# Kernel tuning notes

Measured on AMD Instinct MI355X. Metric: run time of the kernel, lower is better.

The kernel has to match this reference:

```python
import jax, jax.numpy as jnp
import numpy as np
from jax import lax

K = 16      # number of neighbors (init k)
TEMP = 1.0  # softmax temperature (init temp)
DIM = 256   # key/query dim (init dim)


def _compute_omega(s, k, t):
    # s: [*B, N]. Faithful port of the torch loop:
    #   alpha = softmax(s); omega_0 = softmax(alpha/t)
    #   alpha += log(1 - omega_{i-1}); omega_i = softmax(alpha/t)
    alpha0 = jax.nn.softmax(s, axis=-1)

    def step(alpha, _):
        om = jax.nn.softmax(alpha / t, axis=-1)
        return alpha + jnp.log(1.0 - om), om

    _, omegas = lax.scan(step, alpha0, None, length=k)  # [K, *B, N]
    return jnp.moveaxis(omegas, 0, -1)  # [*B, N, K]


def setup_inputs() -> dict:
    key = jax.random.key(0)
    kq, kk, kv = jax.random.split(key, 3)
    B, D, N, F = 8, DIM, 32768, 256
    query = jax.random.normal(kq, (B, D), dtype=jnp.float32)
    keys = jax.random.normal(kk, (B, D, N), dtype=jnp.float32)
    values = jax.random.normal(kv, (B, F, N), dtype=jnp.float32)
    return {"query": query, "keys": keys, "values": values}


def reference(query, keys, values):
    # similarity: -(q . k) / sqrt(D)  -> [B, N]
    sims = -jnp.einsum('bd,bdn->bn', query, keys) / (DIM ** 0.5)
    omega = _compute_omega(sims, K, TEMP)  # [B, N, K]
    # weighted aggregation of values -> [B, K, F]
    k_nearest = jnp.einsum('bnk,bfn->bkf', omega, values)
    return k_nearest
```

## Files before the change

### kernel.cpp

```cpp
#include <hip/hip_runtime.h>

#define B_ 8
#define D_ 256
#define N_ 32768
#define F_ 256
#define K_ 16

__global__ __launch_bounds__(1024) void sims_kernel(
    const float* __restrict__ q, const float* __restrict__ keys,
    float* __restrict__ sims) {
  const int b = blockIdx.x >> 5;
  const int chunk = blockIdx.x & 31;
  const int t = threadIdx.x;
  const int c = t & 255;
  const int g = t >> 8;
  __shared__ float qs[D_];
  __shared__ float4 part[4][256];
  if (t < D_) qs[t] = q[b * D_ + t];
  __syncthreads();
  const int n0 = chunk * 1024 + c * 4;
  const float* kp = keys + (size_t)b * D_ * N_ + (size_t)(g * 64) * N_ + n0;
  const float* qg = qs + g * 64;
  float ax = 0.f, ay = 0.f, az = 0.f, aw = 0.f;
#pragma unroll 8
  for (int d = 0; d < 64; ++d) {
    float4 kv = *reinterpret_cast<const float4*>(kp + (size_t)d * N_);
    float qd = qg[d];
    ax += qd * kv.x; ay += qd * kv.y; az += qd * kv.z; aw += qd * kv.w;
  }
  part[g][c] = make_float4(ax, ay, az, aw);
  __syncthreads();
  if (g == 0) {
    float4 p1 = part[1][c], p2 = part[2][c], p3 = part[3][c];
    float4 o;
    o.x = -0.0625f * (ax + p1.x + p2.x + p3.x);
    o.y = -0.0625f * (ay + p1.y + p2.y + p3.y);
    o.z = -0.0625f * (az + p1.z + p2.z + p3.z);
    o.w = -0.0625f * (aw + p1.w + p2.w + p3.w);
    *reinterpret_cast<float4*>(sims + (size_t)b * N_ + n0) = o;
  }
}

__device__ __forceinline__ float block_allreduce(float v, bool is_max,
                                                 float* red) {
  const int t = threadIdx.x;
#pragma unroll
  for (int off = 32; off > 0; off >>= 1) {
    float o = __shfl_xor(v, off, 64);
    v = is_max ? fmaxf(v, o) : (v + o);
  }
  __syncthreads();
  if ((t & 63) == 0) red[t >> 6] = v;
  __syncthreads();
  if (t == 0) {
    float x = red[0];
#pragma unroll
    for (int w = 1; w < 16; ++w) x = is_max ? fmaxf(x, red[w]) : (x + red[w]);
    red[16] = x;
  }
  __syncthreads();
  return red[16];
}

__global__ __launch_bounds__(1024) void stats_kernel(
    const float* __restrict__ sims, float* __restrict__ om,
    float* __restrict__ qout) {
  const int b = blockIdx.x;
  const int t = threadIdx.x;
  const float* s = sims + (size_t)b * N_;
  float* ob = om + (size_t)b * N_;
  __shared__ float red[17];

  float a[32];
#pragma unroll
  for (int j = 0; j < 32; ++j) a[j] = s[t + j * 1024];

  float m = -1e30f;
#pragma unroll
  for (int j = 0; j < 32; ++j) m = fmaxf(m, a[j]);
  m = block_allreduce(m, true, red);

  float sum = 0.f;
#pragma unroll
  for (int j = 0; j < 32; ++j) { a[j] = __expf(a[j] - m); sum += a[j]; }
  const float invZ1 = 1.0f / block_allreduce(sum, false, red);

  float s1 = 0.f, s2 = 0.f;
#pragma unroll
  for (int j = 0; j < 32; ++j) {
    float f = __expf(a[j] * invZ1);
    a[j] = f;
    s1 += f;
    s2 += f * f;
  }
  const float Z2 = block_allreduce(s1, false, red);
  const float S2 = block_allreduce(s2, false, red);
  const float invZ2 = 1.0f / Z2;
#pragma unroll
  for (int j = 0; j < 32; ++j) ob[t + j * 1024] = a[j] * invZ2;
  if (t == 0) qout[b] = S2 * invZ2 * invZ2;
}

__global__ __launch_bounds__(256) void agg_kernel(
    const float* __restrict__ om, const float* __restrict__ values,
    const float* __restrict__ qarr, float* __restrict__ out) {
  const int b = blockIdx.x & 7;
  const int f0 = (blockIdx.x >> 3) * 4;
  const int t = threadIdx.x;
  const float* ob = om + (size_t)b * N_;
  const float* vb = values + (size_t)b * F_ * N_;

  float A[4] = {0.f, 0.f, 0.f, 0.f};
  float Bv[4] = {0.f, 0.f, 0.f, 0.f};

#pragma unroll 2
  for (int it = 0; it < 32; ++it) {
    const int n0 = (it * 256 + t) * 4;
    float4 o4 = *reinterpret_cast<const float4*>(ob + n0);
    float4 o2;
    o2.x = o4.x * o4.x; o2.y = o4.y * o4.y;
    o2.z = o4.z * o4.z; o2.w = o4.w * o4.w;
#pragma unroll
    for (int f = 0; f < 4; ++f) {
      float4 v4 = *reinterpret_cast<const float4*>(vb + (size_t)(f0 + f) * N_ + n0);
      A[f]  += v4.x * o4.x + v4.y * o4.y + v4.z * o4.z + v4.w * o4.w;
      Bv[f] += v4.x * o2.x + v4.y * o2.y + v4.z * o2.z + v4.w * o2.w;
    }
  }

#pragma unroll
  for (int f = 0; f < 4; ++f) {
#pragma unroll
    for (int off = 32; off > 0; off >>= 1) {
      A[f]  += __shfl_xor(A[f], off, 64);
      Bv[f] += __shfl_xor(Bv[f], off, 64);
    }
  }

  __shared__ float red[4][8];
  const int wid = t >> 6, lane = t & 63;
  if (lane == 0) {
#pragma unroll
    for (int f = 0; f < 4; ++f) { red[wid][f] = A[f]; red[wid][4 + f] = Bv[f]; }
  }
  __syncthreads();
  if (t < 64) {
    const int k = t & 15, fi = t >> 4;
    const float Af = red[0][fi] + red[1][fi] + red[2][fi] + red[3][fi];
    const float Bf = red[0][4 + fi] + red[1][4 + fi] + red[2][4 + fi] + red[3][4 + fi];
    const float qb = qarr[b];
    out[((size_t)b * K_ + k) * F_ + f0 + fi] = Af + (float)k * (qb * Af - Bf);
  }
}

extern "C" void kernel_launch(void* const* d_in, const int* in_sizes, int n_in,
                              void* d_out, int out_size, void* d_ws, size_t ws_size,
                              hipStream_t stream) {
  const float* q = (const float*)d_in[0];
  const float* keys = (const float*)d_in[1];
  const float* values = (const float*)d_in[2];
  float* out = (float*)d_out;
  float* ws = (float*)d_ws;
  float* sims = ws;
  float* om   = ws + (size_t)B_ * N_;
  float* qarr = ws + (size_t)2 * B_ * N_;

  sims_kernel<<<dim3(256), dim3(1024), 0, stream>>>(q, keys, sims);
  stats_kernel<<<dim3(B_), dim3(1024), 0, stream>>>(sims, om, qarr);
  agg_kernel<<<dim3(512), dim3(256), 0, stream>>>(om, values, qarr, out);
}
```

Baseline: 108.7 us.

## Replace softmax stats kernel with Taylor-moment expansion fused into sims and aggregation

Removes the single-block-per-batch stats kernel by computing exp(sims) and its partial moment sums (sum e, e^2, e^3) directly in the similarity kernel. The aggregation kernel accumulates value sums weighted by e^0..e^3 and reconstructs the second softmax and its correction term through a third-order Taylor expansion in double precision. This eliminates the serialized low-parallelism stats pass and one workspace round trip. The trade-off is that accuracy relies on the second-softmax inputs (alpha ~ 1/N) being small enough for the truncated series, and the aggregation does more FMAs per value load.

```diff
diff --git a/kernel.cpp b/kernel.cpp
--- a/kernel.cpp
+++ b/kernel.cpp
@@ -6,19 +6,23 @@
 #define F_ 256
 #define K_ 16
 
-__global__ __launch_bounds__(1024) void sims_kernel(
+
+__device__ __forceinline__ float sum4(float4 v) { return v.x + v.y + v.z + v.w; }
+
+__global__ __launch_bounds__(512) void expsim_kernel(
     const float* __restrict__ q, const float* __restrict__ keys,
-    float* __restrict__ sims) {
-  const int b = blockIdx.x >> 5;
-  const int chunk = blockIdx.x & 31;
+    float* __restrict__ e, float* __restrict__ pp) {
+  const int b = blockIdx.x >> 6;
+  const int chunk = blockIdx.x & 63;
   const int t = threadIdx.x;
-  const int c = t & 255;
-  const int g = t >> 8;
+  const int c = t & 127;
+  const int g = t >> 7;
   __shared__ float qs[D_];
-  __shared__ float4 part[4][256];
+  __shared__ float4 part[3][128];
+  __shared__ float pr[8][3];
   if (t < D_) qs[t] = q[b * D_ + t];
   __syncthreads();
-  const int n0 = chunk * 1024 + c * 4;
+  const int n0 = chunk * 512 + c * 4;
   const float* kp = keys + (size_t)b * D_ * N_ + (size_t)(g * 64) * N_ + n0;
   const float* qg = qs + g * 64;
   float ax = 0.f, ay = 0.f, az = 0.f, aw = 0.f;
@@ -28,128 +32,131 @@
     float qd = qg[d];
     ax += qd * kv.x; ay += qd * kv.y; az += qd * kv.z; aw += qd * kv.w;
   }
-  part[g][c] = make_float4(ax, ay, az, aw);
+  if (g > 0) part[g - 1][c] = make_float4(ax, ay, az, aw);
   __syncthreads();
+  float s1 = 0.f, s2 = 0.f, s3 = 0.f;
   if (g == 0) {
-    float4 p1 = part[1][c], p2 = part[2][c], p3 = part[3][c];
-    float4 o;
-    o.x = -0.0625f * (ax + p1.x + p2.x + p3.x);
-    o.y = -0.0625f * (ay + p1.y + p2.y + p3.y);
-    o.z = -0.0625f * (az + p1.z + p2.z + p3.z);
-    o.w = -0.0625f * (aw + p1.w + p2.w + p3.w);
-    *reinterpret_cast<float4*>(sims + (size_t)b * N_ + n0) = o;
+    float4 p1 = part[0][c], p2 = part[1][c], p3 = part[2][c];
+    float4 ev;
+    ev.x = __expf(-0.0625f * (ax + p1.x + p2.x + p3.x));
+    ev.y = __expf(-0.0625f * (ay + p1.y + p2.y + p3.y));
+    ev.z = __expf(-0.0625f * (az + p1.z + p2.z + p3.z));
+    ev.w = __expf(-0.0625f * (aw + p1.w + p2.w + p3.w));
+    *reinterpret_cast<float4*>(e + (size_t)b * N_ + n0) = ev;
+    float4 e2 = make_float4(ev.x * ev.x, ev.y * ev.y, ev.z * ev.z, ev.w * ev.w);
+    s1 = sum4(ev);
+    s2 = sum4(e2);
+    s3 = e2.x * ev.x + e2.y * ev.y + e2.z * ev.z + e2.w * ev.w;
+  }
+#pragma unroll
+  for (int off = 32; off > 0; off >>= 1) {
+    s1 += __shfl_xor(s1, off, 64);
+    s2 += __shfl_xor(s2, off, 64);
+    s3 += __shfl_xor(s3, off, 64);
+  }
+  if ((t & 63) == 0) { pr[t >> 6][0] = s1; pr[t >> 6][1] = s2; pr[t >> 6][2] = s3; }
+  __syncthreads();
+  if (t == 0) {
+    float r1 = 0.f, r2 = 0.f, r3 = 0.f;
+#pragma unroll
+    for (int w = 0; w < 8; ++w) { r1 += pr[w][0]; r2 += pr[w][1]; r3 += pr[w][2]; }
+    pp[0 * B_ * 64 + b * 64 + chunk] = r1;
+    pp[1 * B_ * 64 + b * 64 + chunk] = r2;
+    pp[2 * B_ * 64 + b * 64 + chunk] = r3;
   }
 }
 
-__device__ __forceinline__ float block_allreduce(float v, bool is_max,
-                                                 float* red) {
+__global__ __launch_bounds__(256, 4) void agg_kernel(
+    const float* __restrict__ e, const float* __restrict__ values,
+    const float* __restrict__ pp, float* __restrict__ out) {
+  const int b = blockIdx.x & 7;
+  const int f0 = (blockIdx.x >> 3) * 2;
   const int t = threadIdx.x;
+  const float* eb = e + (size_t)b * N_;
+  const float* vp0 = values + ((size_t)b * F_ + f0) * N_;
+  const float* vp1 = vp0 + N_;
+
+  float4 a0[2], a1[2], a2[2], a3[2];
 #pragma unroll
-  for (int off = 32; off > 0; off >>= 1) {
-    float o = __shfl_xor(v, off, 64);
-    v = is_max ? fmaxf(v, o) : (v + o);
+  for (int f = 0; f < 2; ++f) {
+    a0[f] = make_float4(0, 0, 0, 0); a1[f] = make_float4(0, 0, 0, 0);
+    a2[f] = make_float4(0, 0, 0, 0); a3[f] = make_float4(0, 0, 0, 0);
   }
-  __syncthreads();
-  if ((t & 63) == 0) red[t >> 6] = v;
-  __syncthreads();
-  if (t == 0) {
-    float x = red[0];
-#pragma unroll
-    for (int w = 1; w < 16; ++w) x = is_max ? fmaxf(x, red[w]) : (x + red[w]);
-    red[16] = x;
-  }
-  __syncthreads();
-  return red[16];
-}
-
-__global__ __launch_bounds__(1024) void stats_kernel(
-    const float* __restrict__ sims, float* __restrict__ om,
-    float* __restrict__ qout) {
-  const int b = blockIdx.x;
-  const int t = threadIdx.x;
-  const float* s = sims + (size_t)b * N_;
-  float* ob = om + (size_t)b * N_;
-  __shared__ float red[17];
-
-  float a[32];
-#pragma unroll
-  for (int j = 0; j < 32; ++j) a[j] = s[t + j * 1024];
-
-  float m = -1e30f;
-#pragma unroll
-  for (int j = 0; j < 32; ++j) m = fmaxf(m, a[j]);
-  m = block_allreduce(m, true, red);
-
-  float sum = 0.f;
-#pragma unroll
-  for (int j = 0; j < 32; ++j) { a[j] = __expf(a[j] - m); sum += a[j]; }
-  const float invZ1 = 1.0f / block_allreduce(sum, false, red);
-
-  float s1 = 0.f, s2 = 0.f;
-#pragma unroll
-  for (int j = 0; j < 32; ++j) {
-    float f = __expf(a[j] * invZ1);
-    a[j] = f;
-    s1 += f;
-    s2 += f * f;
-  }
-  const float Z2 = block_allreduce(s1, false, red);
-  const float S2 = block_allreduce(s2, false, red);
-  const float invZ2 = 1.0f / Z2;
-#pragma unroll
-  for (int j = 0; j < 32; ++j) ob[t + j * 1024] = a[j] * invZ2;
-  if (t == 0) qout[b] = S2 * invZ2 * invZ2;
-}
-
-__global__ __launch_bounds__(256) void agg_kernel(
-    const float* __restrict__ om, const float* __restrict__ values,
-    const float* __restrict__ qarr, float* __restrict__ out) {
-  const int b = blockIdx.x & 7;
-  const int f0 = (blockIdx.x >> 3) * 4;
-  const int t = threadIdx.x;
-  const float* ob = om + (size_t)b * N_;
-  const float* vb = values + (size_t)b * F_ * N_;
-
-  float A[4] = {0.f, 0.f, 0.f, 0.f};
-  float Bv[4] = {0.f, 0.f, 0.f, 0.f};
 
 #pragma unroll 2
   for (int it = 0; it < 32; ++it) {
     const int n0 = (it * 256 + t) * 4;
-    float4 o4 = *reinterpret_cast<const float4*>(ob + n0);
-    float4 o2;
-    o2.x = o4.x * o4.x; o2.y = o4.y * o4.y;
-    o2.z = o4.z * o4.z; o2.w = o4.w * o4.w;
-#pragma unroll
-    for (int f = 0; f < 4; ++f) {
-      float4 v4 = *reinterpret_cast<const float4*>(vb + (size_t)(f0 + f) * N_ + n0);
-      A[f]  += v4.x * o4.x + v4.y * o4.y + v4.z * o4.z + v4.w * o4.w;
-      Bv[f] += v4.x * o2.x + v4.y * o2.y + v4.z * o2.z + v4.w * o2.w;
-    }
+    float4 e1 = *reinterpret_cast<const float4*>(eb + n0);
+    float4 e2 = make_float4(e1.x * e1.x, e1.y * e1.y, e1.z * e1.z, e1.w * e1.w);
+    float4 e3 = make_float4(e2.x * e1.x, e2.y * e1.y, e2.z * e1.z, e2.w * e1.w);
+    float4 va = *reinterpret_cast<const float4*>(vp0 + n0);
+    a0[0].x += va.x;        a0[0].y += va.y;        a0[0].z += va.z;        a0[0].w += va.w;
+    a1[0].x += va.x * e1.x; a1[0].y += va.y * e1.y; a1[0].z += va.z * e1.z; a1[0].w += va.w * e1.w;
+    a2[0].x += va.x * e2.x; a2[0].y += va.y * e2.y; a2[0].z += va.z * e2.z; a2[0].w += va.w * e2.w;
+    a3[0].x += va.x * e3.x; a3[0].y += va.y * e3.y; a3[0].z += va.z * e3.z; a3[0].w += va.w * e3.w;
+    float4 vb = *reinterpret_cast<const float4*>(vp1 + n0);
+    a0[1].x += vb.x;        a0[1].y += vb.y;        a0[1].z += vb.z;        a0[1].w += vb.w;
+    a1[1].x += vb.x * e1.x; a1[1].y += vb.y * e1.y; a1[1].z += vb.z * e1.z; a1[1].w += vb.w * e1.w;
+    a2[1].x += vb.x * e2.x; a2[1].y += vb.y * e2.y; a2[1].z += vb.z * e2.z; a2[1].w += vb.w * e2.w;
+    a3[1].x += vb.x * e3.x; a3[1].y += vb.y * e3.y; a3[1].z += vb.z * e3.z; a3[1].w += vb.w * e3.w;
   }
 
+  float S[8] = {sum4(a0[0]), sum4(a0[1]), sum4(a1[0]), sum4(a1[1]),
+                sum4(a2[0]), sum4(a2[1]), sum4(a3[0]), sum4(a3[1])};
 #pragma unroll
-  for (int f = 0; f < 4; ++f) {
+  for (int i = 0; i < 8; ++i) {
 #pragma unroll
-    for (int off = 32; off > 0; off >>= 1) {
-      A[f]  += __shfl_xor(A[f], off, 64);
-      Bv[f] += __shfl_xor(Bv[f], off, 64);
-    }
+    for (int off = 32; off > 0; off >>= 1) S[i] += __shfl_xor(S[i], off, 64);
   }
-
   __shared__ float red[4][8];
+  __shared__ double dsc[4];
   const int wid = t >> 6, lane = t & 63;
   if (lane == 0) {
 #pragma unroll
-    for (int f = 0; f < 4; ++f) { red[wid][f] = A[f]; red[wid][4 + f] = Bv[f]; }
+    for (int i = 0; i < 8; ++i) red[wid][i] = S[i];
   }
   __syncthreads();
+
   if (t < 64) {
-    const int k = t & 15, fi = t >> 4;
-    const float Af = red[0][fi] + red[1][fi] + red[2][fi] + red[3][fi];
-    const float Bf = red[0][4 + fi] + red[1][4 + fi] + red[2][4 + fi] + red[3][4 + fi];
-    const float qb = qarr[b];
-    out[((size_t)b * K_ + k) * F_ + f0 + fi] = Af + (float)k * (qb * Af - Bf);
+    double z1 = (double)pp[b * 64 + t];
+    double w2 = (double)pp[B_ * 64 + b * 64 + t];
+    double w3 = (double)pp[2 * B_ * 64 + b * 64 + t];
+#pragma unroll
+    for (int off = 32; off > 0; off >>= 1) {
+      z1 += __shfl_xor(z1, off, 64);
+      w2 += __shfl_xor(w2, off, 64);
+      w3 += __shfl_xor(w3, off, 64);
+    }
+    if (t == 0) {
+      double V[8];
+#pragma unroll
+      for (int i = 0; i < 8; ++i)
+        V[i] = (double)red[0][i] + (double)red[1][i] + (double)red[2][i] + (double)red[3][i];
+      const double iZ1 = 1.0 / z1;
+      const double M2 = w2 * iZ1 * iZ1;
+      const double M3 = w3 * iZ1 * iZ1 * iZ1;
+      const double Z2 = (double)N_ + 1.0 + 0.5 * M2 + M3 / 6.0;
+      const double T2 = (double)N_ + 2.0 + 2.0 * M2 + (4.0 / 3.0) * M3;
+      const double iZ2 = 1.0 / Z2;
+      const double qd = T2 * iZ2 * iZ2;
+#pragma unroll
+      for (int f = 0; f < 2; ++f) {
+        const double W0 = V[f];
+        const double W1 = V[2 + f] * iZ1;
+        const double W2 = V[4 + f] * iZ1 * iZ1;
+        const double W3 = V[6 + f] * iZ1 * iZ1 * iZ1;
+        const double A  = (W0 + W1 + 0.5 * W2 + W3 / 6.0) * iZ2;
+        const double Bd = (W0 + 2.0 * W1 + 2.0 * W2 + (4.0 / 3.0) * W3) * iZ2 * iZ2;
+        dsc[f * 2]     = A;
+        dsc[f * 2 + 1] = qd * A - Bd;
+      }
+    }
+  }
+  __syncthreads();
+  if (t < 32) {
+    const int k = t & 15, f = t >> 4;
+    const double A = dsc[f * 2], C = dsc[f * 2 + 1];
+    out[((size_t)b * K_ + k) * F_ + f0 + f] = (float)(A + (double)k * C);
   }
 }
 
@@ -161,11 +168,9 @@
   const float* values = (const float*)d_in[2];
   float* out = (float*)d_out;
   float* ws = (float*)d_ws;
-  float* sims = ws;
-  float* om   = ws + (size_t)B_ * N_;
-  float* qarr = ws + (size_t)2 * B_ * N_;
+  float* e = ws;
+  float* pp = ws + (size_t)B_ * N_;
 
-  sims_kernel<<<dim3(256), dim3(1024), 0, stream>>>(q, keys, sims);
-  stats_kernel<<<dim3(B_), dim3(1024), 0, stream>>>(sims, om, qarr);
-  agg_kernel<<<dim3(512), dim3(256), 0, stream>>>(om, values, qarr, out);
+  expsim_kernel<<<dim3(512), dim3(512), 0, stream>>>(q, keys, e, pp);
+  agg_kernel<<<dim3(1024), dim3(256), 0, stream>>>(e, values, pp, out);
 }
```

Result: no change. 109.7 us (+0.9%).
